# Optimization experiments

Measured on AMD Instinct MI355X. Metric: run time of the kernel, lower is better.

## Reference

```python
import jax, jax.numpy as jnp
import numpy as np

N_EXPERTS = 8
N_ACTIVE = 2


def setup_inputs() -> dict:
    key = jax.random.key(0)
    k0, k1, k2, k3, k4 = jax.random.split(key, 5)
    B, S, D, H, E = 4, 2048, 1024, 2816, N_EXPERTS
    return {
        "x": jax.random.normal(k0, (B, S, D), dtype=jnp.float32),
        "Wr": jax.random.normal(k1, (D, E), dtype=jnp.float32) * 0.02,
        "w1": jax.random.normal(k2, (E, D, H), dtype=jnp.float32) * 0.02,
        "w3": jax.random.normal(k3, (E, D, H), dtype=jnp.float32) * 0.02,
        "w2": jax.random.normal(k4, (E, H, D), dtype=jnp.float32) * 0.02,
    }


def reference(x, Wr, w1, w3, w2):
    B, S, D = x.shape
    E, K = N_EXPERTS, N_ACTIVE
    xf = x.reshape(-1, D)  # (T, D), T = B*S

    # --- Router: top-k over softmax probs, renormalized weights ---
    logits = xf @ Wr                       # (T, E)
    probs = jax.nn.softmax(logits, axis=-1)
    topk_vals, topk_idx = jax.lax.top_k(probs, K)   # (T, K)
    topk_w = topk_vals / jnp.sum(topk_vals, axis=-1, keepdims=True)

    # combine weight per (token, expert): sum of slot weights routed to expert
    onehot = jax.nn.one_hot(topk_idx, E, dtype=xf.dtype)  # (T, K, E)
    combine = jnp.einsum('tk,tke->te', topk_w, onehot)    # (T, E)

    # --- Load-balancing aux loss: E * sum_e f_e * P_e ---
    f = onehot.mean(axis=(0, 1))     # fraction of (token,slot) assignments per expert
    P = probs.mean(axis=0)           # mean router prob per expert
    aux_loss = E * jnp.sum(f * P)

    # --- Experts: SwiGLU, combined with router weights (zero weight = unrouted) ---
    out = jnp.zeros_like(xf)
    for e in range(E):  # small fixed expert count
        h = jax.nn.silu(xf @ w1[e]) * (xf @ w3[e])  # (T, H)
        out = out + combine[:, e:e + 1] * (h @ w2[e])
    return out.reshape(B, S, D), aux_loss
```

## Files before the change

kernel.cpp:

```cpp
#include <hip/hip_runtime.h>
#include <hip/hip_bf16.h>
#include <stdint.h>


#define T_TOK 8192
#define D_DIM 1024
#define H_DIM 2816
#define E_EXP 8
#define NSLOT 16384
#define CAP_ROWS 18432
#define MT1_MAX 72
#define MT2_MAX 136

#define MI_T1 0
#define MI_T2 1
#define MI_POS 8
#define MI_MTE1 16
#define MI_MTB1 (16 + MT1_MAX)
#define MI_MTE2 (16 + 2 * MT1_MAX)
#define MI_MTB2 (16 + 2 * MT1_MAX + MT2_MAX)

typedef __attribute__((ext_vector_type(8))) short short8;
typedef __attribute__((ext_vector_type(4))) float f32x4;

#define GLD16(gsrc, ldst) __builtin_amdgcn_global_load_lds( \
    (const __attribute__((address_space(1))) void*)(gsrc),  \
    (__attribute__((address_space(3))) void*)(ldst), 16, 0, 0)

__global__ __launch_bounds__(256) void transpose_all(const float* __restrict__ w1,
                                                     const float* __restrict__ w3,
                                                     const float* __restrict__ w2,
                                                     __hip_bfloat16* __restrict__ w13t,
                                                     __hip_bfloat16* __restrict__ w2t) {
  __shared__ float tile[64][65];
  int bid = blockIdx.x, tid = threadIdx.x;
  int lc = (tid & 15) * 4;
  int lr = tid >> 4;
  if (bid < 11264) {
    int z = bid / 704, rem = bid % 704;
    int bx = rem % 44, by = rem / 44;
    int e = z >> 1, w3f = z & 1;
    const float* in = w3f ? w3 : w1;
    int h0 = bx * 64, d0 = by * 64;
    const float* src = in + ((size_t)e * D_DIM + d0) * H_DIM + h0;
#pragma unroll
    for (int i = 0; i < 4; i++) {
      float4 v = *(const float4*)(src + (size_t)(lr + i * 16) * H_DIM + lc);
      tile[lr + i * 16][lc + 0] = v.x;
      tile[lr + i * 16][lc + 1] = v.y;
      tile[lr + i * 16][lc + 2] = v.z;
      tile[lr + i * 16][lc + 3] = v.w;
    }
    __syncthreads();
    __hip_bfloat16* dstE = w13t + (size_t)e * (2 * H_DIM) * D_DIM;
    int rB = (tid & 7) * 8;
#pragma unroll
    for (int i = 0; i < 2; i++) {
      int hh = (tid >> 3) + i * 32;
      int habs = h0 + hh;
      int rw = 2 * (habs & ~15) + (habs & 15) + (w3f ? 16 : 0);
      __align__(16) __hip_bfloat16 o[8];
#pragma unroll
      for (int k = 0; k < 8; k++) o[k] = __float2bfloat16(tile[rB + k][hh]);
      *(short8*)(dstE + (size_t)rw * D_DIM + d0 + rB) = *(const short8*)o;
    }
  } else {
    int b2 = bid - 11264;
    int e = b2 / 704, rem = b2 % 704;
    int bx = rem % 16, by = rem / 16;
    int c0 = bx * 64, r0 = by * 64;
    const float* src = w2 + ((size_t)e * H_DIM + r0) * D_DIM + c0;
#pragma unroll
    for (int i = 0; i < 4; i++) {
      float4 v = *(const float4*)(src + (size_t)(lr + i * 16) * D_DIM + lc);
      tile[lr + i * 16][lc + 0] = v.x;
      tile[lr + i * 16][lc + 1] = v.y;
      tile[lr + i * 16][lc + 2] = v.z;
      tile[lr + i * 16][lc + 3] = v.w;
    }
    __syncthreads();
    __hip_bfloat16* dst = w2t + ((size_t)e * D_DIM + c0) * H_DIM + r0;
    int rB = (tid & 7) * 8;
#pragma unroll
    for (int i = 0; i < 2; i++) {
      int c = (tid >> 3) + i * 32;
      __align__(16) __hip_bfloat16 o[8];
#pragma unroll
      for (int k = 0; k < 8; k++) o[k] = __float2bfloat16(tile[rB + k][c]);
      *(short8*)(dst + (size_t)c * H_DIM + rB) = *(const short8*)o;
    }
  }
}

__global__ __launch_bounds__(256) void router_kernel(const float* __restrict__ x,
                                                     const float* __restrict__ Wr,
                                                     float* __restrict__ Pbuf,
                                                     int* __restrict__ expert_sel,
                                                     float* __restrict__ slot_w) {
  int wave = threadIdx.x >> 6, lane = threadIdx.x & 63;
  int tok = blockIdx.x * 4 + wave;
  const float* xr = x + (size_t)tok * D_DIM;
  float acc[8];
#pragma unroll
  for (int e = 0; e < 8; e++) acc[e] = 0.f;
  for (int d = lane; d < D_DIM; d += 64) {
    float xv = xr[d];
    const float4* w4 = (const float4*)(Wr + d * 8);
    float4 wa = w4[0], wb = w4[1];
    acc[0] += xv * wa.x; acc[1] += xv * wa.y; acc[2] += xv * wa.z; acc[3] += xv * wa.w;
    acc[4] += xv * wb.x; acc[5] += xv * wb.y; acc[6] += xv * wb.z; acc[7] += xv * wb.w;
  }
#pragma unroll
  for (int e = 0; e < 8; e++) {
#pragma unroll
    for (int off = 32; off >= 1; off >>= 1) acc[e] += __shfl_xor(acc[e], off);
  }
  float mx = acc[0];
#pragma unroll
  for (int e = 1; e < 8; e++) mx = fmaxf(mx, acc[e]);
  float p[8], s = 0.f;
#pragma unroll
  for (int e = 0; e < 8; e++) { p[e] = expf(acc[e] - mx); s += p[e]; }
  float inv = 1.f / s;
#pragma unroll
  for (int e = 0; e < 8; e++) p[e] *= inv;
  int i0 = 0;
#pragma unroll
  for (int e = 1; e < 8; e++) if (p[e] > p[i0]) i0 = e;
  int i1 = (i0 == 0) ? 1 : 0;
#pragma unroll
  for (int e = 0; e < 8; e++) if (e != i0 && p[e] > p[i1]) i1 = e;
  float wsum = p[i0] + p[i1];

  __shared__ float sP[4][8];
  if (lane == 0) {
    expert_sel[tok * 2] = i0;
    expert_sel[tok * 2 + 1] = i1;
    slot_w[tok * 2] = p[i0] / wsum;
    slot_w[tok * 2 + 1] = p[i1] / wsum;
#pragma unroll
    for (int e = 0; e < 8; e++) sP[wave][e] = p[e];
  }
  __syncthreads();
  if (threadIdx.x < 8)
    Pbuf[threadIdx.x * 2048 + blockIdx.x] =
        sP[0][threadIdx.x] + sP[1][threadIdx.x] + sP[2][threadIdx.x] + sP[3][threadIdx.x];
}

__global__ __launch_bounds__(256) void offsets_kernel(const int* __restrict__ expert_sel,
                                                      int* __restrict__ meta,
                                                      const float* __restrict__ Pbuf,
                                                      float* __restrict__ aux_out) {
  int t = threadIdx.x;
  unsigned long long pA = 0, pB = 0;
  for (int i = 0; i < 64; i++) {
    int e = expert_sel[i * 256 + t];
    if (e < 4) pA += 1ull << (e * 16);
    else       pB += 1ull << ((e - 4) * 16);
  }
#pragma unroll
  for (int off = 32; off >= 1; off >>= 1) {
    pA += __shfl_xor(pA, off);
    pB += __shfl_xor(pB, off);
  }
  __shared__ unsigned long long sA[4], sB[4];
  __shared__ float red[8][33];
  int wave = t >> 6, lane = t & 63;
  if (lane == 0) { sA[wave] = pA; sB[wave] = pB; }
  int ee = t >> 5, j = t & 31;
  float s = 0.f;
  for (int c = j; c < 2048; c += 32) s += Pbuf[ee * 2048 + c];
  red[ee][j] = s;
  __syncthreads();
  if (t == 0) {
    unsigned long long A = sA[0] + sA[1] + sA[2] + sA[3];
    unsigned long long B = sB[0] + sB[1] + sB[2] + sB[3];
    int cnt[8];
    for (int e = 0; e < 4; e++) cnt[e] = (int)((A >> (e * 16)) & 0xFFFF);
    for (int e = 0; e < 4; e++) cnt[4 + e] = (int)((B >> (e * 16)) & 0xFFFF);
    float psum[8];
    for (int e = 0; e < 8; e++) {
      float ss = 0.f;
      for (int k = 0; k < 32; k++) ss += red[e][k];
      psum[e] = ss;
    }
    int off = 0, n1 = 0, n2 = 0;
    float aux = 0.f;
    for (int e = 0; e < 8; e++) {
      int c = cnt[e];
      meta[MI_POS + e] = off;
      int t1 = (c + 255) >> 8;
      for (int jj = 0; jj < t1; jj++) { meta[MI_MTE1 + n1] = e; meta[MI_MTB1 + n1] = off + jj * 256; n1++; }
      int t2 = (c + 127) >> 7;
      for (int jj = 0; jj < t2; jj++) { meta[MI_MTE2 + n2] = e; meta[MI_MTB2 + n2] = off + jj * 128; n2++; }
      off += t1 * 256;
      aux += ((float)c / 16384.f) * (psum[e] / 8192.f);
    }
    meta[MI_T1] = n1;
    meta[MI_T2] = n2;
    *aux_out = 8.f * aux;
  }
}

__global__ __launch_bounds__(256) void assign_kernel(const int* __restrict__ expert_sel,
                                                     int* __restrict__ meta,
                                                     int* __restrict__ slot_pos) {
  int tid = threadIdx.x, wave = tid >> 6, lane = tid & 63;
  int slot = blockIdx.x * 256 + tid;
  int e = expert_sel[slot];
  __shared__ int cnt[4][8];
  __shared__ int base[8];
  __shared__ int woff[4][8];
  int rank = 0;
#pragma unroll
  for (int ee = 0; ee < 8; ee++) {
    unsigned long long msk = __ballot(e == ee);
    if (lane == 0) cnt[wave][ee] = __popcll(msk);
    if (e == ee) rank = __popcll(msk & ((1ull << lane) - 1ull));
  }
  __syncthreads();
  if (tid < 8) {
    int c0 = cnt[0][tid], c1 = cnt[1][tid], c2 = cnt[2][tid], c3 = cnt[3][tid];
    int tot = c0 + c1 + c2 + c3;
    base[tid] = atomicAdd(&meta[MI_POS + tid], tot);
    woff[0][tid] = 0; woff[1][tid] = c0; woff[2][tid] = c0 + c1; woff[3][tid] = c0 + c1 + c2;
  }
  __syncthreads();
  slot_pos[slot] = base[e] + woff[wave][e] + rank;
}

__global__ __launch_bounds__(256) void gather_kernel(const int* __restrict__ slot_pos,
                                                     const float* __restrict__ x,
                                                     __hip_bfloat16* __restrict__ Xg) {
  int wave = threadIdx.x >> 6, lane = threadIdx.x & 63;
  int tok = blockIdx.x * 4 + wave;
  int p0 = slot_pos[tok * 2], p1 = slot_pos[tok * 2 + 1];
  const float4* src = (const float4*)(x + (size_t)tok * D_DIM);
  __hip_bfloat16* d0 = Xg + (size_t)p0 * D_DIM;
  __hip_bfloat16* d1 = Xg + (size_t)p1 * D_DIM;
#pragma unroll
  for (int p = 0; p < 4; p++) {
    float4 v = src[p * 64 + lane];
    union { ushort4 u4; __hip_bfloat16 h[4]; } cv;
    cv.h[0] = __float2bfloat16(v.x);
    cv.h[1] = __float2bfloat16(v.y);
    cv.h[2] = __float2bfloat16(v.z);
    cv.h[3] = __float2bfloat16(v.w);
    *(ushort4*)(d0 + (p * 64 + lane) * 4) = cv.u4;
    *(ushort4*)(d1 + (p * 64 + lane) * 4) = cv.u4;
  }
}

__device__ __forceinline__ short8 frag_read64(const char* tile, int row, int gk) {
  int byte = (row << 7) | ((gk ^ (row & 7)) << 4);
  return *(const short8*)(tile + byte);
}

template <int NITER, int BLK>
__device__ __forceinline__ void stage_rowsT(const __hip_bfloat16* gbase, int ld, char* tile,
                                            int tid) {
#pragma unroll
  for (int i = 0; i < NITER; i++) {
    int L = i * (BLK * 16) + tid * 16;
    int row = L >> 7;
    int g = (L >> 4) & 7;
    int gs = g ^ (row & 7);
    const char* src = (const char*)(gbase + (size_t)row * ld) + gs * 16;
    GLD16(src, tile + i * (BLK * 16) + (tid >> 6) * 1024);
  }
}

__device__ __forceinline__ void tile_from_bid(int bid, int nwg, int mmax, int* m, int* n) {
  int cpx = nwg >> 3;
  int u = (bid & 7) * cpx + (bid >> 3);
  *n = u / mmax;
  *m = u % mmax;
}

__global__ __launch_bounds__(256, 2) void gemm1_kernel(const __hip_bfloat16* __restrict__ Xg,
                                                       const __hip_bfloat16* __restrict__ w13t,
                                                       __hip_bfloat16* __restrict__ Hb,
                                                       const int* __restrict__ meta) {
  int m, nIdx;
  tile_from_bid(blockIdx.x, (2 * H_DIM / 256) * MT2_MAX, MT2_MAX, &m, &nIdx);
  if (m >= meta[MI_T2]) return;
  int e = meta[MI_MTE2 + m];
  int row0 = meta[MI_MTB2 + m];
  int n0 = nIdx * 256;
  __shared__ __align__(16) char ldsA[16384];
  __shared__ __align__(16) char ldsB[32768];
  int tid = threadIdx.x, wave = tid >> 6, lane = tid & 63;
  int wr = wave >> 1, wc = wave & 1;
  const __hip_bfloat16* Ab = Xg + (size_t)row0 * D_DIM;
  const __hip_bfloat16* Bb = w13t + ((size_t)e * (2 * H_DIM) + n0) * D_DIM;

  f32x4 acc[4][8];
#pragma unroll
  for (int i = 0; i < 4; i++)
#pragma unroll
    for (int j = 0; j < 8; j++) acc[i][j] = 0.f;

  int rsel = lane & 15, kg = lane >> 4;
  for (int k0 = 0; k0 < D_DIM; k0 += 64) {
    stage_rowsT<4, 256>(Ab + k0, D_DIM, ldsA, tid);
    stage_rowsT<8, 256>(Bb + k0, D_DIM, ldsB, tid);
    asm volatile("s_waitcnt vmcnt(0)" ::: "memory");
    __syncthreads();
#pragma unroll
    for (int kk = 0; kk < 2; kk++) {
      int gk = kk * 4 + kg;
      short8 a[4], b[8];
#pragma unroll
      for (int f = 0; f < 4; f++) a[f] = frag_read64(ldsA, wr * 64 + f * 16 + rsel, gk);
#pragma unroll
      for (int f = 0; f < 8; f++) b[f] = frag_read64(ldsB, wc * 128 + f * 16 + rsel, gk);
#pragma unroll
      for (int fm = 0; fm < 4; fm++)
#pragma unroll
        for (int fn = 0; fn < 8; fn++)
          acc[fm][fn] = __builtin_amdgcn_mfma_f32_16x16x32_bf16(a[fm], b[fn], acc[fm][fn], 0, 0, 0);
    }
    __syncthreads();
  }
  int rq = lane >> 4;
#pragma unroll
  for (int fm = 0; fm < 4; fm++)
#pragma unroll
    for (int fnp = 0; fnp < 4; fnp++)
#pragma unroll
      for (int j = 0; j < 4; j++) {
        float v1 = acc[fm][2 * fnp][j], v3 = acc[fm][2 * fnp + 1][j];
        float h = (v1 / (1.f + expf(-v1))) * v3;
        int r = row0 + wr * 64 + fm * 16 + rq * 4 + j;
        int c = (n0 >> 1) + wc * 64 + fnp * 16 + rsel;
        Hb[(size_t)r * H_DIM + c] = __float2bfloat16(h);
      }
}

__global__ __launch_bounds__(256, 2) void gemm2_kernel(const __hip_bfloat16* __restrict__ Hb,
                                                       const __hip_bfloat16* __restrict__ w2t,
                                                       __hip_bfloat16* __restrict__ Y,
                                                       const int* __restrict__ meta) {
  int m, nIdx;
  tile_from_bid(blockIdx.x, (D_DIM / 256) * MT2_MAX, MT2_MAX, &m, &nIdx);
  if (m >= meta[MI_T2]) return;
  int e = meta[MI_MTE2 + m];
  int row0 = meta[MI_MTB2 + m];
  int n0 = nIdx * 256;
  __shared__ __align__(16) char ldsA[16384];
  __shared__ __align__(16) char ldsB[32768];
  int tid = threadIdx.x, wave = tid >> 6, lane = tid & 63;
  int wr = wave >> 1, wc = wave & 1;
  const __hip_bfloat16* Ab = Hb + (size_t)row0 * H_DIM;
  const __hip_bfloat16* Bb = w2t + ((size_t)e * D_DIM + n0) * H_DIM;

  f32x4 acc[4][8];
#pragma unroll
  for (int i = 0; i < 4; i++)
#pragma unroll
    for (int j = 0; j < 8; j++) acc[i][j] = 0.f;

  int rsel = lane & 15, kg = lane >> 4;
  for (int k0 = 0; k0 < H_DIM; k0 += 64) {
    stage_rowsT<4, 256>(Ab + k0, H_DIM, ldsA, tid);
    stage_rowsT<8, 256>(Bb + k0, H_DIM, ldsB, tid);
    asm volatile("s_waitcnt vmcnt(0)" ::: "memory");
    __syncthreads();
#pragma unroll
    for (int kk = 0; kk < 2; kk++) {
      int gk = kk * 4 + kg;
      short8 a[4], b[8];
#pragma unroll
      for (int f = 0; f < 4; f++) a[f] = frag_read64(ldsA, wr * 64 + f * 16 + rsel, gk);
#pragma unroll
      for (int f = 0; f < 8; f++) b[f] = frag_read64(ldsB, wc * 128 + f * 16 + rsel, gk);
#pragma unroll
      for (int fm = 0; fm < 4; fm++)
#pragma unroll
        for (int fn = 0; fn < 8; fn++)
          acc[fm][fn] = __builtin_amdgcn_mfma_f32_16x16x32_bf16(a[fm], b[fn], acc[fm][fn], 0, 0, 0);
    }
    __syncthreads();
  }
  int rq = lane >> 4;
#pragma unroll
  for (int fm = 0; fm < 4; fm++)
#pragma unroll
    for (int fn = 0; fn < 8; fn++)
#pragma unroll
      for (int j = 0; j < 4; j++) {
        int r = row0 + wr * 64 + fm * 16 + rq * 4 + j;
        int c = n0 + wc * 128 + fn * 16 + rsel;
        Y[(size_t)r * D_DIM + c] = __float2bfloat16(acc[fm][fn][j]);
      }
}

__global__ __launch_bounds__(256) void combine_kernel(const int* __restrict__ slot_pos,
                                                      const float* __restrict__ slot_w,
                                                      const __hip_bfloat16* __restrict__ Y,
                                                      float* __restrict__ outp) {
  int tok = blockIdx.x;
  int p0 = slot_pos[tok * 2], p1 = slot_pos[tok * 2 + 1];
  float w0 = slot_w[tok * 2], w1 = slot_w[tok * 2 + 1];
  int i4 = threadIdx.x;
  ushort4 a = *(const ushort4*)(Y + (size_t)p0 * D_DIM + i4 * 4);
  ushort4 b = *(const ushort4*)(Y + (size_t)p1 * D_DIM + i4 * 4);
  union { ushort u; __hip_bfloat16 h; } c0, c1;
  float4 r;
  c0.u = a.x; c1.u = b.x; r.x = w0 * __bfloat162float(c0.h) + w1 * __bfloat162float(c1.h);
  c0.u = a.y; c1.u = b.y; r.y = w0 * __bfloat162float(c0.h) + w1 * __bfloat162float(c1.h);
  c0.u = a.z; c1.u = b.z; r.z = w0 * __bfloat162float(c0.h) + w1 * __bfloat162float(c1.h);
  c0.u = a.w; c1.u = b.w; r.w = w0 * __bfloat162float(c0.h) + w1 * __bfloat162float(c1.h);
  ((float4*)(outp + (size_t)tok * D_DIM))[i4] = r;
}

extern "C" void kernel_launch(void* const* d_in, const int* in_sizes, int n_in,
                              void* d_out, int out_size, void* d_ws, size_t ws_size,
                              hipStream_t stream) {
  const float* x = (const float*)d_in[0];
  const float* Wr = (const float*)d_in[1];
  const float* w1 = (const float*)d_in[2];
  const float* w3 = (const float*)d_in[3];
  const float* w2 = (const float*)d_in[4];
  float* outp = (float*)d_out;

  char* ws = (char*)d_ws;
  size_t off = 0;
  auto alloc = [&](size_t bytes) -> char* {
    char* p = ws + off;
    off += (bytes + 255) & ~(size_t)255;
    return p;
  };
  __hip_bfloat16* w13t = (__hip_bfloat16*)alloc((size_t)E_EXP * 2 * H_DIM * D_DIM * 2);
  __hip_bfloat16* w2t = (__hip_bfloat16*)alloc((size_t)E_EXP * D_DIM * H_DIM * 2);
  __hip_bfloat16* Xg = (__hip_bfloat16*)alloc((size_t)CAP_ROWS * D_DIM * 2);
  __hip_bfloat16* Hb = (__hip_bfloat16*)alloc((size_t)CAP_ROWS * H_DIM * 2);
  __hip_bfloat16* Y = (__hip_bfloat16*)alloc((size_t)CAP_ROWS * D_DIM * 2);
  float* slot_w = (float*)alloc(NSLOT * 4);
  int* slot_pos = (int*)alloc(NSLOT * 4);
  int* expert_sel = (int*)alloc(NSLOT * 4);
  float* Pbuf = (float*)alloc(2048 * 8 * 4);
  int* meta = (int*)alloc(2048);
  (void)ws_size; (void)in_sizes; (void)n_in; (void)out_size;

  transpose_all<<<dim3(16896), dim3(256), 0, stream>>>(w1, w3, w2, w13t, w2t);
  router_kernel<<<dim3(T_TOK / 4), dim3(256), 0, stream>>>(x, Wr, Pbuf, expert_sel, slot_w);
  offsets_kernel<<<dim3(1), dim3(256), 0, stream>>>(expert_sel, meta, Pbuf, outp + (size_t)T_TOK * D_DIM);
  assign_kernel<<<dim3(NSLOT / 256), dim3(256), 0, stream>>>(expert_sel, meta, slot_pos);
  gather_kernel<<<dim3(T_TOK / 4), dim3(256), 0, stream>>>(slot_pos, x, Xg);
  gemm1_kernel<<<dim3((2 * H_DIM / 256) * MT2_MAX), dim3(256), 0, stream>>>(Xg, w13t, Hb, meta);
  gemm2_kernel<<<dim3((D_DIM / 256) * MT2_MAX), dim3(256), 0, stream>>>(Hb, w2t, Y, meta);
  combine_kernel<<<dim3(T_TOK), dim3(256), 0, stream>>>(slot_pos, slot_w, Y, outp);
}
```

Before: 556.2 us.

## Fuse router into transpose, combine into GEMM2 via atomics, pad experts to 128

The router computation moves into the weight-transpose launch as extra blocks, saving one launch. The combine step is folded into the GEMM2 epilogue: each output row is scaled by its routing weight and atomically added into a zero-initialised fp32 output, using new position-to-token and position-to-weight maps. This removes the bf16 Y buffer and the separate combine kernel. Expert segments are now padded to 128-row multiples instead of 256, which reduces padded rows in both GEMMs. In exchange there are two memsets and many scattered fp32 global atomics, which may be costly, especially if they compile to compare-and-swap loops.

```diff
diff --git a/kernel.cpp b/kernel.cpp
--- a/kernel.cpp
+++ b/kernel.cpp
@@ -9,16 +9,12 @@
 #define E_EXP 8
 #define NSLOT 16384
 #define CAP_ROWS 18432
-#define MT1_MAX 72
-#define MT2_MAX 136
-
-#define MI_T1 0
+#define MT_MAX 136
+
 #define MI_T2 1
 #define MI_POS 8
-#define MI_MTE1 16
-#define MI_MTB1 (16 + MT1_MAX)
-#define MI_MTE2 (16 + 2 * MT1_MAX)
-#define MI_MTB2 (16 + 2 * MT1_MAX + MT2_MAX)
+#define MI_MTE2 16
+#define MI_MTB2 (16 + MT_MAX)
 
 typedef __attribute__((ext_vector_type(8))) short short8;
 typedef __attribute__((ext_vector_type(4))) float f32x4;
@@ -27,12 +23,18 @@
     (const __attribute__((address_space(1))) void*)(gsrc),  \
     (__attribute__((address_space(3))) void*)(ldst), 16, 0, 0)
 
-__global__ __launch_bounds__(256) void transpose_all(const float* __restrict__ w1,
-                                                     const float* __restrict__ w3,
-                                                     const float* __restrict__ w2,
-                                                     __hip_bfloat16* __restrict__ w13t,
-                                                     __hip_bfloat16* __restrict__ w2t) {
+__global__ __launch_bounds__(256) void transpose_router(const float* __restrict__ w1,
+                                                        const float* __restrict__ w3,
+                                                        const float* __restrict__ w2,
+                                                        __hip_bfloat16* __restrict__ w13t,
+                                                        __hip_bfloat16* __restrict__ w2t,
+                                                        const float* __restrict__ x,
+                                                        const float* __restrict__ Wr,
+                                                        float* __restrict__ Pbuf,
+                                                        int* __restrict__ expert_sel,
+                                                        float* __restrict__ slot_w) {
   __shared__ float tile[64][65];
+  __shared__ float sP[4][8];
   int bid = blockIdx.x, tid = threadIdx.x;
   int lc = (tid & 15) * 4;
   int lr = tid >> 4;
@@ -64,7 +66,7 @@
       for (int k = 0; k < 8; k++) o[k] = __float2bfloat16(tile[rB + k][hh]);
       *(short8*)(dstE + (size_t)rw * D_DIM + d0 + rB) = *(const short8*)o;
     }
-  } else {
+  } else if (bid < 16896) {
     int b2 = bid - 11264;
     int e = b2 / 704, rem = b2 % 704;
     int bx = rem % 16, by = rem / 16;
@@ -89,62 +91,54 @@
       for (int k = 0; k < 8; k++) o[k] = __float2bfloat16(tile[rB + k][c]);
       *(short8*)(dst + (size_t)c * H_DIM + rB) = *(const short8*)o;
     }
-  }
-}
-
-__global__ __launch_bounds__(256) void router_kernel(const float* __restrict__ x,
-                                                     const float* __restrict__ Wr,
-                                                     float* __restrict__ Pbuf,
-                                                     int* __restrict__ expert_sel,
-                                                     float* __restrict__ slot_w) {
-  int wave = threadIdx.x >> 6, lane = threadIdx.x & 63;
-  int tok = blockIdx.x * 4 + wave;
-  const float* xr = x + (size_t)tok * D_DIM;
-  float acc[8];
-#pragma unroll
-  for (int e = 0; e < 8; e++) acc[e] = 0.f;
-  for (int d = lane; d < D_DIM; d += 64) {
-    float xv = xr[d];
-    const float4* w4 = (const float4*)(Wr + d * 8);
-    float4 wa = w4[0], wb = w4[1];
-    acc[0] += xv * wa.x; acc[1] += xv * wa.y; acc[2] += xv * wa.z; acc[3] += xv * wa.w;
-    acc[4] += xv * wb.x; acc[5] += xv * wb.y; acc[6] += xv * wb.z; acc[7] += xv * wb.w;
-  }
-#pragma unroll
-  for (int e = 0; e < 8; e++) {
-#pragma unroll
-    for (int off = 32; off >= 1; off >>= 1) acc[e] += __shfl_xor(acc[e], off);
-  }
-  float mx = acc[0];
-#pragma unroll
-  for (int e = 1; e < 8; e++) mx = fmaxf(mx, acc[e]);
-  float p[8], s = 0.f;
-#pragma unroll
-  for (int e = 0; e < 8; e++) { p[e] = expf(acc[e] - mx); s += p[e]; }
-  float inv = 1.f / s;
-#pragma unroll
-  for (int e = 0; e < 8; e++) p[e] *= inv;
-  int i0 = 0;
-#pragma unroll
-  for (int e = 1; e < 8; e++) if (p[e] > p[i0]) i0 = e;
-  int i1 = (i0 == 0) ? 1 : 0;
-#pragma unroll
-  for (int e = 0; e < 8; e++) if (e != i0 && p[e] > p[i1]) i1 = e;
-  float wsum = p[i0] + p[i1];
-
-  __shared__ float sP[4][8];
-  if (lane == 0) {
-    expert_sel[tok * 2] = i0;
-    expert_sel[tok * 2 + 1] = i1;
-    slot_w[tok * 2] = p[i0] / wsum;
-    slot_w[tok * 2 + 1] = p[i1] / wsum;
-#pragma unroll
-    for (int e = 0; e < 8; e++) sP[wave][e] = p[e];
-  }
-  __syncthreads();
-  if (threadIdx.x < 8)
-    Pbuf[threadIdx.x * 2048 + blockIdx.x] =
-        sP[0][threadIdx.x] + sP[1][threadIdx.x] + sP[2][threadIdx.x] + sP[3][threadIdx.x];
+  } else {
+    int rb = bid - 16896;
+    int wave = tid >> 6, lane = tid & 63;
+    int tok = rb * 4 + wave;
+    const float* xr = x + (size_t)tok * D_DIM;
+    float acc[8];
+#pragma unroll
+    for (int e = 0; e < 8; e++) acc[e] = 0.f;
+    for (int d = lane; d < D_DIM; d += 64) {
+      float xv = xr[d];
+      const float4* w4 = (const float4*)(Wr + d * 8);
+      float4 wa = w4[0], wb = w4[1];
+      acc[0] += xv * wa.x; acc[1] += xv * wa.y; acc[2] += xv * wa.z; acc[3] += xv * wa.w;
+      acc[4] += xv * wb.x; acc[5] += xv * wb.y; acc[6] += xv * wb.z; acc[7] += xv * wb.w;
+    }
+#pragma unroll
+    for (int e = 0; e < 8; e++) {
+#pragma unroll
+      for (int off = 32; off >= 1; off >>= 1) acc[e] += __shfl_xor(acc[e], off);
+    }
+    float mx = acc[0];
+#pragma unroll
+    for (int e = 1; e < 8; e++) mx = fmaxf(mx, acc[e]);
+    float p[8], s = 0.f;
+#pragma unroll
+    for (int e = 0; e < 8; e++) { p[e] = expf(acc[e] - mx); s += p[e]; }
+    float inv = 1.f / s;
+#pragma unroll
+    for (int e = 0; e < 8; e++) p[e] *= inv;
+    int i0 = 0;
+#pragma unroll
+    for (int e = 1; e < 8; e++) if (p[e] > p[i0]) i0 = e;
+    int i1 = (i0 == 0) ? 1 : 0;
+#pragma unroll
+    for (int e = 0; e < 8; e++) if (e != i0 && p[e] > p[i1]) i1 = e;
+    float wsum = p[i0] + p[i1];
+    if (lane == 0) {
+      expert_sel[tok * 2] = i0;
+      expert_sel[tok * 2 + 1] = i1;
+      slot_w[tok * 2] = p[i0] / wsum;
+      slot_w[tok * 2 + 1] = p[i1] / wsum;
+#pragma unroll
+      for (int e = 0; e < 8; e++) sP[wave][e] = p[e];
+    }
+    __syncthreads();
+    if (tid < 8)
+      Pbuf[tid * 2048 + rb] = sP[0][tid] + sP[1][tid] + sP[2][tid] + sP[3][tid];
+  }
 }
 
 __global__ __launch_bounds__(256) void offsets_kernel(const int* __restrict__ expert_sel,
@@ -184,27 +178,27 @@
       for (int k = 0; k < 32; k++) ss += red[e][k];
       psum[e] = ss;
     }
-    int off = 0, n1 = 0, n2 = 0;
+    int off = 0, n2 = 0;
     float aux = 0.f;
     for (int e = 0; e < 8; e++) {
       int c = cnt[e];
       meta[MI_POS + e] = off;
-      int t1 = (c + 255) >> 8;
-      for (int jj = 0; jj < t1; jj++) { meta[MI_MTE1 + n1] = e; meta[MI_MTB1 + n1] = off + jj * 256; n1++; }
       int t2 = (c + 127) >> 7;
       for (int jj = 0; jj < t2; jj++) { meta[MI_MTE2 + n2] = e; meta[MI_MTB2 + n2] = off + jj * 128; n2++; }
-      off += t1 * 256;
+      off += t2 * 128;
       aux += ((float)c / 16384.f) * (psum[e] / 8192.f);
     }
-    meta[MI_T1] = n1;
     meta[MI_T2] = n2;
     *aux_out = 8.f * aux;
   }
 }
 
 __global__ __launch_bounds__(256) void assign_kernel(const int* __restrict__ expert_sel,
+                                                     const float* __restrict__ slot_w,
                                                      int* __restrict__ meta,
-                                                     int* __restrict__ slot_pos) {
+                                                     int* __restrict__ slot_pos,
+                                                     int* __restrict__ tok_of_pos,
+                                                     float* __restrict__ w_of_pos) {
   int tid = threadIdx.x, wave = tid >> 6, lane = tid & 63;
   int slot = blockIdx.x * 256 + tid;
   int e = expert_sel[slot];
@@ -226,7 +220,10 @@
     woff[0][tid] = 0; woff[1][tid] = c0; woff[2][tid] = c0 + c1; woff[3][tid] = c0 + c1 + c2;
   }
   __syncthreads();
-  slot_pos[slot] = base[e] + woff[wave][e] + rank;
+  int pos = base[e] + woff[wave][e] + rank;
+  slot_pos[slot] = pos;
+  tok_of_pos[pos] = slot >> 1;
+  w_of_pos[pos] = slot_w[slot];
 }
 
 __global__ __launch_bounds__(256) void gather_kernel(const int* __restrict__ slot_pos,
@@ -282,7 +279,7 @@
                                                        __hip_bfloat16* __restrict__ Hb,
                                                        const int* __restrict__ meta) {
   int m, nIdx;
-  tile_from_bid(blockIdx.x, (2 * H_DIM / 256) * MT2_MAX, MT2_MAX, &m, &nIdx);
+  tile_from_bid(blockIdx.x, (2 * H_DIM / 256) * MT_MAX, MT_MAX, &m, &nIdx);
   if (m >= meta[MI_T2]) return;
   int e = meta[MI_MTE2 + m];
   int row0 = meta[MI_MTB2 + m];
@@ -339,10 +336,12 @@
 
 __global__ __launch_bounds__(256, 2) void gemm2_kernel(const __hip_bfloat16* __restrict__ Hb,
                                                        const __hip_bfloat16* __restrict__ w2t,
-                                                       __hip_bfloat16* __restrict__ Y,
+                                                       const int* __restrict__ tok_of_pos,
+                                                       const float* __restrict__ w_of_pos,
+                                                       float* __restrict__ outp,
                                                        const int* __restrict__ meta) {
   int m, nIdx;
-  tile_from_bid(blockIdx.x, (D_DIM / 256) * MT2_MAX, MT2_MAX, &m, &nIdx);
+  tile_from_bid(blockIdx.x, (D_DIM / 256) * MT_MAX, MT_MAX, &m, &nIdx);
   if (m >= meta[MI_T2]) return;
   int e = meta[MI_MTE2 + m];
   int row0 = meta[MI_MTB2 + m];
@@ -386,32 +385,18 @@
 #pragma unroll
   for (int fm = 0; fm < 4; fm++)
 #pragma unroll
-    for (int fn = 0; fn < 8; fn++)
-#pragma unroll
-      for (int j = 0; j < 4; j++) {
-        int r = row0 + wr * 64 + fm * 16 + rq * 4 + j;
+    for (int j = 0; j < 4; j++) {
+      int r = row0 + wr * 64 + fm * 16 + rq * 4 + j;
+      int tok = tok_of_pos[r];
+      if (tok < 0) continue;
+      float w = w_of_pos[r];
+      float* orow = outp + (size_t)tok * D_DIM;
+#pragma unroll
+      for (int fn = 0; fn < 8; fn++) {
         int c = n0 + wc * 128 + fn * 16 + rsel;
-        Y[(size_t)r * D_DIM + c] = __float2bfloat16(acc[fm][fn][j]);
+        atomicAdd(&orow[c], w * acc[fm][fn][j]);
       }
-}
-
-__global__ __launch_bounds__(256) void combine_kernel(const int* __restrict__ slot_pos,
-                                                      const float* __restrict__ slot_w,
-                                                      const __hip_bfloat16* __restrict__ Y,
-                                                      float* __restrict__ outp) {
-  int tok = blockIdx.x;
-  int p0 = slot_pos[tok * 2], p1 = slot_pos[tok * 2 + 1];
-  float w0 = slot_w[tok * 2], w1 = slot_w[tok * 2 + 1];
-  int i4 = threadIdx.x;
-  ushort4 a = *(const ushort4*)(Y + (size_t)p0 * D_DIM + i4 * 4);
-  ushort4 b = *(const ushort4*)(Y + (size_t)p1 * D_DIM + i4 * 4);
-  union { ushort u; __hip_bfloat16 h; } c0, c1;
-  float4 r;
-  c0.u = a.x; c1.u = b.x; r.x = w0 * __bfloat162float(c0.h) + w1 * __bfloat162float(c1.h);
-  c0.u = a.y; c1.u = b.y; r.y = w0 * __bfloat162float(c0.h) + w1 * __bfloat162float(c1.h);
-  c0.u = a.z; c1.u = b.z; r.z = w0 * __bfloat162float(c0.h) + w1 * __bfloat162float(c1.h);
-  c0.u = a.w; c1.u = b.w; r.w = w0 * __bfloat162float(c0.h) + w1 * __bfloat162float(c1.h);
-  ((float4*)(outp + (size_t)tok * D_DIM))[i4] = r;
+    }
 }
 
 extern "C" void kernel_launch(void* const* d_in, const int* in_sizes, int n_in,
@@ -435,20 +420,25 @@
   __hip_bfloat16* w2t = (__hip_bfloat16*)alloc((size_t)E_EXP * D_DIM * H_DIM * 2);
   __hip_bfloat16* Xg = (__hip_bfloat16*)alloc((size_t)CAP_ROWS * D_DIM * 2);
   __hip_bfloat16* Hb = (__hip_bfloat16*)alloc((size_t)CAP_ROWS * H_DIM * 2);
-  __hip_bfloat16* Y = (__hip_bfloat16*)alloc((size_t)CAP_ROWS * D_DIM * 2);
   float* slot_w = (float*)alloc(NSLOT * 4);
   int* slot_pos = (int*)alloc(NSLOT * 4);
   int* expert_sel = (int*)alloc(NSLOT * 4);
+  int* tok_of_pos = (int*)alloc(CAP_ROWS * 4);
+  float* w_of_pos = (float*)alloc(CAP_ROWS * 4);
   float* Pbuf = (float*)alloc(2048 * 8 * 4);
   int* meta = (int*)alloc(2048);
-  (void)ws_size; (void)in_sizes; (void)n_in; (void)out_size;
-
-  transpose_all<<<dim3(16896), dim3(256), 0, stream>>>(w1, w3, w2, w13t, w2t);
-  router_kernel<<<dim3(T_TOK / 4), dim3(256), 0, stream>>>(x, Wr, Pbuf, expert_sel, slot_w);
+  (void)ws_size; (void)in_sizes; (void)n_in;
+
+  hipMemsetAsync(outp, 0, (size_t)out_size * 4, stream);
+  hipMemsetAsync(tok_of_pos, 0xFF, (size_t)CAP_ROWS * 4, stream);
+
+  transpose_router<<<dim3(18944), dim3(256), 0, stream>>>(w1, w3, w2, w13t, w2t,
+                                                          x, Wr, Pbuf, expert_sel, slot_w);
   offsets_kernel<<<dim3(1), dim3(256), 0, stream>>>(expert_sel, meta, Pbuf, outp + (size_t)T_TOK * D_DIM);
-  assign_kernel<<<dim3(NSLOT / 256), dim3(256), 0, stream>>>(expert_sel, meta, slot_pos);
+  assign_kernel<<<dim3(NSLOT / 256), dim3(256), 0, stream>>>(expert_sel, slot_w, meta, slot_pos,
+                                                             tok_of_pos, w_of_pos);
   gather_kernel<<<dim3(T_TOK / 4), dim3(256), 0, stream>>>(slot_pos, x, Xg);
-  gemm1_kernel<<<dim3((2 * H_DIM / 256) * MT2_MAX), dim3(256), 0, stream>>>(Xg, w13t, Hb, meta);
-  gemm2_kernel<<<dim3((D_DIM / 256) * MT2_MAX), dim3(256), 0, stream>>>(Hb, w2t, Y, meta);
-  combine_kernel<<<dim3(T_TOK), dim3(256), 0, stream>>>(slot_pos, slot_w, Y, outp);
-}
+  gemm1_kernel<<<dim3((2 * H_DIM / 256) * MT_MAX), dim3(256), 0, stream>>>(Xg, w13t, Hb, meta);
+  gemm2_kernel<<<dim3((D_DIM / 256) * MT_MAX), dim3(256), 0, stream>>>(Hb, w2t, tok_of_pos,
+                                                                       w_of_pos, outp, meta);
+}
```

Result: slower. 593.0 us (+6.6%).
